# Performance work log

Measured on AMD Instinct MI355X. Metric: run time of the kernel, lower is better.

Reference implementation:

```python
import jax, jax.numpy as jnp
import numpy as np
from jax import lax

B, C, H, W = 8, 96, 192, 192
HEADS = 3
FFN = 2 * C  # chn_expanded * in_channels
EPS = 1e-6


def layernorm2d(x, w, b):
    # channel-mean LayerNorm over dim 1 (NCHW)
    mu = jnp.mean(x, axis=1, keepdims=True)
    var = jnp.mean((x - mu) ** 2, axis=1, keepdims=True)
    y = (x - mu) / jnp.sqrt(var + EPS)
    return w[None, :, None, None] * y + b[None, :, None, None]


def conv1x1(x, w, b):
    # w: [out, in]
    return jnp.einsum('bchw,oc->bohw', x, w) + b[None, :, None, None]


def dwconv3x3(x, w, b):
    # depthwise 3x3, w: [C3, 1, 3, 3]
    y = lax.conv_general_dilated(x, w, (1, 1), 'SAME',
                                 feature_group_count=x.shape[1],
                                 dimension_numbers=('NCHW', 'OIHW', 'NCHW'))
    return y + b[None, :, None, None]


def l2norm(x):
    n = jnp.sqrt(jnp.sum(x * x, axis=-1, keepdims=True))
    return x / jnp.maximum(n, 1e-12)


def setup_inputs() -> dict:
    key = jax.random.key(0)
    ks = jax.random.split(key, 10)
    s = 1.0 / np.sqrt(C)
    return {
        'x': jax.random.normal(ks[0], (B, C, H, W), jnp.float32),
        'ln1_w': jnp.ones((C,), jnp.float32),
        'ln1_b': jnp.zeros((C,), jnp.float32),
        'ln2_w': jnp.ones((C,), jnp.float32),
        'ln2_b': jnp.zeros((C,), jnp.float32),
        'qkv_w': jax.random.normal(ks[1], (3 * C, C), jnp.float32) * s,
        'qkv_b': jnp.zeros((3 * C,), jnp.float32),
        'dw_w': jax.random.normal(ks[2], (3 * C, 1, 3, 3), jnp.float32) * 0.1,
        'dw_b': jnp.zeros((3 * C,), jnp.float32),
        'temp': jnp.ones((HEADS, 1, 1), jnp.float32),
        'proj_w': jax.random.normal(ks[3], (C, C), jnp.float32) * s,
        'proj_b': jnp.zeros((C,), jnp.float32),
        'conv1_w': jax.random.normal(ks[4], (FFN, C), jnp.float32) * s,
        'conv1_b': jnp.zeros((FFN,), jnp.float32),
        'conv2_w': jax.random.normal(ks[5], (C, FFN // 2), jnp.float32) * s,
        'conv2_b': jnp.zeros((C,), jnp.float32),
        'betac': jax.random.normal(ks[6], (1, C, 1, 1), jnp.float32) * 0.1,
        'gamma': jax.random.normal(ks[7], (1, C, 1, 1), jnp.float32) * 0.1,
    }


def channel_attn(qkv, temp, proj_w, proj_b):
    b, c3, h, w = qkv.shape
    q, k, v = jnp.split(qkv, 3, axis=1)
    def r(t):  # b (head c) h w -> b head c (h w)
        return t.reshape(b, HEADS, C // HEADS, h * w)
    q, k, v = r(q), r(k), r(v)
    q = l2norm(q)
    k = l2norm(k)
    attn = jnp.einsum('bhcn,bhdn->bhcd', q, k) * temp[None]  # [b,head,c,c]
    attn = jax.nn.softmax(jax.nn.relu(attn), axis=-1)
    out = jnp.einsum('bhcd,bhdn->bhcn', attn, v)
    out = out.reshape(b, C, h, w)
    return conv1x1(out, proj_w, proj_b)


def reference(x, ln1_w, ln1_b, ln2_w, ln2_b, qkv_w, qkv_b, dw_w, dw_b, temp,
              proj_w, proj_b, conv1_w, conv1_b, conv2_w, conv2_b, betac, gamma):
    xn = layernorm2d(x, ln1_w, ln1_b)
    qkv = dwconv3x3(conv1x1(xn, qkv_w, qkv_b), dw_w, dw_b)
    xc = channel_attn(qkv, temp, proj_w, proj_b)
    y = x + xc * betac
    f = conv1x1(layernorm2d(y, ln2_w, ln2_b), conv1_w, conv1_b)
    f1, f2 = jnp.split(f, 2, axis=1)
    f = conv1x1(f1 * f2, conv2_w, conv2_b)
    return y + f * gamma
```

## Files before the change

### kernel.cpp

```cpp
#include <hip/hip_runtime.h>

#define BB 8
#define C 96
#define HH 192
#define WW 192
#define NPIX (HH*WW)
#define C3 (3*C)
#define NHEADS 3
#define FFND 192
#define EPSV 1e-6f
#define PT 64
#define GNB 768

typedef unsigned short u16;
typedef unsigned int u32;
typedef __attribute__((ext_vector_type(8))) short bf16x8;
typedef __attribute__((ext_vector_type(4))) float f32x4;

__device__ __forceinline__ float b2f(u16 h) {
  u32 u = ((u32)h) << 16;
  return __builtin_bit_cast(float, u);
}
__device__ __forceinline__ u16 f2b(float f) {
  u32 u = __builtin_bit_cast(u32, f);
  u32 r = (u + 0x7FFFu + ((u >> 16) & 1u)) >> 16;
  return (u16)r;
}
__device__ __forceinline__ u32 pk2(float a, float b) {
  return (u32)f2b(a) | ((u32)f2b(b) << 16);
}


__global__ __launch_bounds__(256) void k_prep(
    const float* __restrict__ qkvw, const float* __restrict__ pw,
    const float* __restrict__ c1w, const float* __restrict__ c2w,
    u16* __restrict__ Wf)
{
  int t = blockIdx.x * 256 + threadIdx.x;
  const float* src; u16* dst; int tl;
  if (t < 3456)      { src = qkvw; dst = Wf;         tl = t; }
  else if (t < 4608) { src = pw;   dst = Wf + 27648; tl = t - 3456; }
  else if (t < 6912) { src = c1w;  dst = Wf + 36864; tl = t - 4608; }
  else if (t < 8064) { src = c2w;  dst = Wf + 55296; tl = t - 6912; }
  else return;
  int fid = tl >> 6, lane = tl & 63;
  int mt = fid / 3, kt = fid % 3;
  int row = mt * 16 + (lane & 15), k0 = kt * 32 + (lane >> 4) * 8;
  const float* s = src + row * 96 + k0;
  uint4 v;
  v.x = pk2(s[0], s[1]); v.y = pk2(s[2], s[3]);
  v.z = pk2(s[4], s[5]); v.w = pk2(s[6], s[7]);
  *reinterpret_cast<uint4*>(dst + (size_t)tl * 8) = v;
}

__global__ __launch_bounds__(256) void k_ln1_qkv(
    const float* __restrict__ x, const float* __restrict__ ln1w,
    const float* __restrict__ ln1b, const u16* __restrict__ Wf,
    const float* __restrict__ qb, u16* __restrict__ qkv_pre, int b0)
{
  __shared__ float xs[C][PT + 1];
  __shared__ __align__(16) u16 xt[PT][104];
  __shared__ float mu_s[PT], rs_s[PT];
  __shared__ float lw[C], lb[C];
  const int tid = threadIdx.x;
  const int nt = NPIX / PT;
  const int bl = blockIdx.x / nt;
  const int tile = blockIdx.x % nt;
  const int n0 = tile * PT;
  const float* xb = x + (size_t)(b0 + bl) * C * NPIX + n0;
  for (int i = tid; i < C * PT; i += 256) {
    int c = i >> 6, p = i & 63;
    xs[c][p] = xb[(size_t)c * NPIX + p];
  }
  if (tid < C) { lw[tid] = ln1w[tid]; lb[tid] = ln1b[tid]; }
  __syncthreads();
  float* red = (float*)xt;
  {
    int g = tid >> 6, p = tid & 63;
    float s = 0.f, ss = 0.f;
    for (int c = g * 24; c < g * 24 + 24; c++) { float v = xs[c][p]; s += v; ss += v * v; }
    red[g * 64 + p] = s; red[(4 + g) * 64 + p] = ss;
  }
  __syncthreads();
  if (tid < PT) {
    float s  = red[tid] + red[64 + tid] + red[128 + tid] + red[192 + tid];
    float ss = red[256 + tid] + red[320 + tid] + red[384 + tid] + red[448 + tid];
    float m = s * (1.f / C);
    float var = ss * (1.f / C) - m * m;
    mu_s[tid] = m; rs_s[tid] = rsqrtf(var + EPSV);
  }
  __syncthreads();
  for (int i = tid; i < C * PT; i += 256) {
    int c = i >> 6, p = i & 63;
    xt[p][c] = f2b((xs[c][p] - mu_s[p]) * rs_s[p] * lw[c] + lb[c]);
  }
  __syncthreads();
  const int lane = tid & 63, wv = tid >> 6;
  const int lr = lane & 15, lg = lane >> 4;
  const int pcol = wv * 16 + lr;
  bf16x8 bf[3];
  #pragma unroll
  for (int kt = 0; kt < 3; kt++)
    bf[kt] = *reinterpret_cast<const bf16x8*>(&xt[pcol][kt * 32 + lg * 8]);
  const bf16x8* wfp = reinterpret_cast<const bf16x8*>(Wf);
  u16* outb = qkv_pre + (size_t)bl * C3 * NPIX + n0 + pcol;
  for (int mt = 0; mt < 18; mt++) {
    f32x4 acc = {0.f, 0.f, 0.f, 0.f};
    #pragma unroll
    for (int kt = 0; kt < 3; kt++)
      acc = __builtin_amdgcn_mfma_f32_16x16x32_bf16(wfp[(mt * 3 + kt) * 64 + lane], bf[kt], acc, 0, 0, 0);
    #pragma unroll
    for (int r = 0; r < 4; r++) {
      int o = mt * 16 + lg * 4 + r;
      outb[(size_t)o * NPIX] = f2b(acc[r] + qb[o]);
    }
  }
}

__global__ __launch_bounds__(256) void k_dwconv(
    const u16* __restrict__ src, const float* __restrict__ dww,
    const float* __restrict__ dwb, u16* __restrict__ dst)
{
  long qid = (long)blockIdx.x * 256 + threadIdx.x;
  int wq = (int)(qid % 48);
  long t = qid / 48;
  int h = (int)(t % HH); t /= HH;
  int ch = (int)(t % C3);
  int bl = (int)(t / C3);
  const u16* p = src + ((size_t)bl * C3 + ch) * NPIX;
  float wgt[9];
  #pragma unroll
  for (int i = 0; i < 9; i++) wgt[i] = dww[ch * 9 + i];
  float acc0 = 0.f, acc1 = 0.f, acc2 = 0.f, acc3 = 0.f;
  int w0 = wq * 4;
  #pragma unroll
  for (int dh = -1; dh <= 1; dh++) {
    int hh = h + dh;
    if (hh < 0 || hh >= HH) continue;
    const u16* row = p + (size_t)hh * WW;
    ushort4 v4 = *reinterpret_cast<const ushort4*>(row + w0);
    float r0 = (w0 > 0) ? b2f(row[w0 - 1]) : 0.f;
    float r1 = b2f(v4.x), r2 = b2f(v4.y), r3 = b2f(v4.z), r4v = b2f(v4.w);
    float r5 = (w0 + 4 < WW) ? b2f(row[w0 + 4]) : 0.f;
    float wA = wgt[(dh + 1) * 3 + 0];
    float wB = wgt[(dh + 1) * 3 + 1];
    float wC = wgt[(dh + 1) * 3 + 2];
    acc0 += r0 * wA + r1 * wB + r2 * wC;
    acc1 += r1 * wA + r2 * wB + r3 * wC;
    acc2 += r2 * wA + r3 * wB + r4v * wC;
    acc3 += r3 * wA + r4v * wB + r5 * wC;
  }
  float bb = dwb[ch];
  ushort4 o4;
  o4.x = f2b(acc0 + bb); o4.y = f2b(acc1 + bb);
  o4.z = f2b(acc2 + bb); o4.w = f2b(acc3 + bb);
  *reinterpret_cast<ushort4*>(dst + ((size_t)bl * C3 + ch) * NPIX + (size_t)h * WW + w0) = o4;
}

__global__ __launch_bounds__(256) void k_gram(
    const u16* __restrict__ qkv, float* __restrict__ G,
    float* __restrict__ nq, float* __restrict__ nk, int b0)
{
  __shared__ float gred[4][1024];
  const int tid = threadIdx.x, lane = tid & 63, wv = tid >> 6;
  const int nch = NPIX / GNB;
  const int bhl = blockIdx.x / nch;
  const int chunk = blockIdx.x % nch;
  const int bl = bhl / NHEADS, hd = bhl % NHEADS;
  const int bh = (b0 + bl) * NHEADS + hd;
  const int lr = lane & 15, lg = lane >> 4;
  const u16* qb_ = qkv + ((size_t)bl * C3 + hd * 32) * NPIX;
  const u16* kb_ = qkv + ((size_t)bl * C3 + C + hd * 32) * NPIX;
  const int nbase = chunk * GNB + wv * (GNB / 4);
  f32x4 a00 = {0,0,0,0}, a01 = {0,0,0,0}, a10 = {0,0,0,0}, a11 = {0,0,0,0};
  float sq0 = 0.f, sq1 = 0.f, sk0 = 0.f, sk1 = 0.f;
  #pragma unroll 2
  for (int it = 0; it < GNB / 4 / 32; it++) {
    int n = nbase + it * 32 + lg * 8;
    bf16x8 fa0 = *reinterpret_cast<const bf16x8*>(qb_ + (size_t)lr * NPIX + n);
    bf16x8 fa1 = *reinterpret_cast<const bf16x8*>(qb_ + (size_t)(16 + lr) * NPIX + n);
    bf16x8 fb0 = *reinterpret_cast<const bf16x8*>(kb_ + (size_t)lr * NPIX + n);
    bf16x8 fb1 = *reinterpret_cast<const bf16x8*>(kb_ + (size_t)(16 + lr) * NPIX + n);
    a00 = __builtin_amdgcn_mfma_f32_16x16x32_bf16(fa0, fb0, a00, 0, 0, 0);
    a01 = __builtin_amdgcn_mfma_f32_16x16x32_bf16(fa0, fb1, a01, 0, 0, 0);
    a10 = __builtin_amdgcn_mfma_f32_16x16x32_bf16(fa1, fb0, a10, 0, 0, 0);
    a11 = __builtin_amdgcn_mfma_f32_16x16x32_bf16(fa1, fb1, a11, 0, 0, 0);
    #pragma unroll
    for (int j = 0; j < 8; j++) {
      float q0 = b2f((u16)fa0[j]), q1 = b2f((u16)fa1[j]);
      float k0 = b2f((u16)fb0[j]), k1 = b2f((u16)fb1[j]);
      sq0 += q0 * q0; sq1 += q1 * q1; sk0 += k0 * k0; sk1 += k1 * k1;
    }
  }
  #pragma unroll
  for (int r = 0; r < 4; r++) {
    gred[wv][(0  + lg * 4 + r) * 32 + 0  + lr] = a00[r];
    gred[wv][(0  + lg * 4 + r) * 32 + 16 + lr] = a01[r];
    gred[wv][(16 + lg * 4 + r) * 32 + 0  + lr] = a10[r];
    gred[wv][(16 + lg * 4 + r) * 32 + 16 + lr] = a11[r];
  }
  sq0 += __shfl_xor(sq0, 16); sq0 += __shfl_xor(sq0, 32);
  sq1 += __shfl_xor(sq1, 16); sq1 += __shfl_xor(sq1, 32);
  sk0 += __shfl_xor(sk0, 16); sk0 += __shfl_xor(sk0, 32);
  sk1 += __shfl_xor(sk1, 16); sk1 += __shfl_xor(sk1, 32);
  if (lg == 0) {
    atomicAdd(&nq[bh * 32 + lr], sq0);
    atomicAdd(&nq[bh * 32 + 16 + lr], sq1);
    atomicAdd(&nk[bh * 32 + lr], sk0);
    atomicAdd(&nk[bh * 32 + 16 + lr], sk1);
  }
  __syncthreads();
  for (int i = tid; i < 1024; i += 256) {
    float s = gred[0][i] + gred[1][i] + gred[2][i] + gred[3][i];
    atomicAdd(&G[(size_t)bh * 1024 + i], s);
  }
}

__global__ void k_softmax(const float* __restrict__ G, const float* __restrict__ nq,
                          const float* __restrict__ nk, const float* __restrict__ temp,
                          u16* __restrict__ Af, int b0)
{
  int bh = b0 * NHEADS + blockIdx.x;
  int c = threadIdx.x;
  int hd = bh % NHEADS;
  float tmp = temp[hd];
  float nqc = fmaxf(sqrtf(nq[bh * 32 + c]), 1e-12f);
  float a[32];
  float m = 0.f;
  #pragma unroll
  for (int d = 0; d < 32; d++) {
    float nkd = fmaxf(sqrtf(nk[bh * 32 + d]), 1e-12f);
    float v = G[(size_t)bh * 1024 + c * 32 + d] / (nqc * nkd) * tmp;
    v = fmaxf(v, 0.f);
    a[d] = v; m = fmaxf(m, v);
  }
  float s = 0.f;
  #pragma unroll
  for (int d = 0; d < 32; d++) { a[d] = expf(a[d] - m); s += a[d]; }
  float inv = 1.f / s;
  #pragma unroll
  for (int lg = 0; lg < 4; lg++) {
    uint4 v;
    v.x = pk2(a[8 * lg + 0] * inv, a[8 * lg + 1] * inv);
    v.y = pk2(a[8 * lg + 2] * inv, a[8 * lg + 3] * inv);
    v.z = pk2(a[8 * lg + 4] * inv, a[8 * lg + 5] * inv);
    v.w = pk2(a[8 * lg + 6] * inv, a[8 * lg + 7] * inv);
    *reinterpret_cast<uint4*>(Af + ((size_t)(bh * 2 + (c >> 4)) * 64 + lg * 16 + (c & 15)) * 8) = v;
  }
}

__global__ __launch_bounds__(256) void k_av_proj(
    const u16* __restrict__ qkv, const u16* __restrict__ Af,
    const u16* __restrict__ pWf, const float* __restrict__ pb,
    const float* __restrict__ x, const float* __restrict__ betac,
    float* __restrict__ y, int b0)
{
  __shared__ __align__(16) u16 vt[PT][104];
  __shared__ __align__(16) u16 avt[PT][104];
  const int tid = threadIdx.x;
  const int nt = NPIX / PT;
  const int bl = blockIdx.x / nt;
  const int tile = blockIdx.x % nt;
  const int b = b0 + bl;
  const int n0 = tile * PT;
  const u16* vb = qkv + ((size_t)bl * C3 + 2 * C) * NPIX + n0;
  for (int i = tid; i < C * PT; i += 256) {
    int c = i >> 6, p = i & 63;
    vt[p][c] = vb[(size_t)c * NPIX + p];
  }
  __syncthreads();
  const int lane = tid & 63, wv = tid >> 6;
  const int lr = lane & 15, lg = lane >> 4;
  const int pcol = wv * 16 + lr;
  const bf16x8* afp = reinterpret_cast<const bf16x8*>(Af);
  #pragma unroll
  for (int h = 0; h < NHEADS; h++) {
    bf16x8 bv = *reinterpret_cast<const bf16x8*>(&vt[pcol][h * 32 + lg * 8]);
    #pragma unroll
    for (int mt = 0; mt < 2; mt++) {
      f32x4 acc = {0.f, 0.f, 0.f, 0.f};
      acc = __builtin_amdgcn_mfma_f32_16x16x32_bf16(
          afp[((size_t)(b * NHEADS + h) * 2 + mt) * 64 + lane], bv, acc, 0, 0, 0);
      int o = h * 32 + mt * 16 + lg * 4;
      u32* dst = reinterpret_cast<u32*>(&avt[pcol][o]);
      dst[0] = pk2(acc[0], acc[1]);
      dst[1] = pk2(acc[2], acc[3]);
    }
  }
  bf16x8 ba[3];
  #pragma unroll
  for (int kt = 0; kt < 3; kt++)
    ba[kt] = *reinterpret_cast<const bf16x8*>(&avt[pcol][kt * 32 + lg * 8]);
  const bf16x8* pwp = reinterpret_cast<const bf16x8*>(pWf);
  const float* xb = x + (size_t)b * C * NPIX + n0 + pcol;
  float* yb = y + (size_t)b * C * NPIX + n0 + pcol;
  for (int mt = 0; mt < 6; mt++) {
    f32x4 acc = {0.f, 0.f, 0.f, 0.f};
    #pragma unroll
    for (int kt = 0; kt < 3; kt++)
      acc = __builtin_amdgcn_mfma_f32_16x16x32_bf16(pwp[(mt * 3 + kt) * 64 + lane], ba[kt], acc, 0, 0, 0);
    #pragma unroll
    for (int r = 0; r < 4; r++) {
      int o = mt * 16 + lg * 4 + r;
      yb[(size_t)o * NPIX] = xb[(size_t)o * NPIX] + (acc[r] + pb[o]) * betac[o];
    }
  }
}

__global__ __launch_bounds__(256) void k_ffn(
    float* __restrict__ y, const float* __restrict__ ln2w,
    const float* __restrict__ ln2b, const u16* __restrict__ c1f,
    const u16* __restrict__ c2f, const float* __restrict__ c1b,
    const float* __restrict__ c2b, const float* __restrict__ gamma)
{
  __shared__ float xs[C][PT + 1];
  __shared__ __align__(16) u16 yt[PT][104];
  __shared__ __align__(16) u16 gt[PT][104];
  __shared__ float mu_s[PT], rs_s[PT];
  __shared__ float lw[C], lb[C];
  const int tid = threadIdx.x;
  const int nt = NPIX / PT;
  const int b = blockIdx.x / nt;
  const int tile = blockIdx.x % nt;
  const int n0 = tile * PT;
  float* yb = y + (size_t)b * C * NPIX + n0;
  for (int i = tid; i < C * PT; i += 256) {
    int c = i >> 6, p = i & 63;
    xs[c][p] = yb[(size_t)c * NPIX + p];
  }
  if (tid < C) { lw[tid] = ln2w[tid]; lb[tid] = ln2b[tid]; }
  __syncthreads();
  float* red = (float*)yt;
  {
    int g = tid >> 6, p = tid & 63;
    float s = 0.f, ss = 0.f;
    for (int c = g * 24; c < g * 24 + 24; c++) { float v = xs[c][p]; s += v; ss += v * v; }
    red[g * 64 + p] = s; red[(4 + g) * 64 + p] = ss;
  }
  __syncthreads();
  if (tid < PT) {
    float s  = red[tid] + red[64 + tid] + red[128 + tid] + red[192 + tid];
    float ss = red[256 + tid] + red[320 + tid] + red[384 + tid] + red[448 + tid];
    float m = s * (1.f / C);
    float var = ss * (1.f / C) - m * m;
    mu_s[tid] = m; rs_s[tid] = rsqrtf(var + EPSV);
  }
  __syncthreads();
  for (int i = tid; i < C * PT; i += 256) {
    int c = i >> 6, p = i & 63;
    yt[p][c] = f2b((xs[c][p] - mu_s[p]) * rs_s[p] * lw[c] + lb[c]);
  }
  __syncthreads();
  const int lane = tid & 63, wv = tid >> 6;
  const int lr = lane & 15, lg = lane >> 4;
  const int pcol = wv * 16 + lr;
  bf16x8 by[3];
  #pragma unroll
  for (int kt = 0; kt < 3; kt++)
    by[kt] = *reinterpret_cast<const bf16x8*>(&yt[pcol][kt * 32 + lg * 8]);
  const bf16x8* w1 = reinterpret_cast<const bf16x8*>(c1f);
  const bf16x8* w2 = reinterpret_cast<const bf16x8*>(c2f);
  for (int mt = 0; mt < 6; mt++) {
    f32x4 a1 = {0.f, 0.f, 0.f, 0.f}, a2 = {0.f, 0.f, 0.f, 0.f};
    #pragma unroll
    for (int kt = 0; kt < 3; kt++) {
      a1 = __builtin_amdgcn_mfma_f32_16x16x32_bf16(w1[(mt * 3 + kt) * 64 + lane], by[kt], a1, 0, 0, 0);
      a2 = __builtin_amdgcn_mfma_f32_16x16x32_bf16(w1[((mt + 6) * 3 + kt) * 64 + lane], by[kt], a2, 0, 0, 0);
    }
    int o = mt * 16 + lg * 4;
    float g0 = (a1[0] + c1b[o + 0]) * (a2[0] + c1b[o + 96]);
    float g1 = (a1[1] + c1b[o + 1]) * (a2[1] + c1b[o + 97]);
    float g2 = (a1[2] + c1b[o + 2]) * (a2[2] + c1b[o + 98]);
    float g3 = (a1[3] + c1b[o + 3]) * (a2[3] + c1b[o + 99]);
    u32* dst = reinterpret_cast<u32*>(&gt[pcol][o]);
    dst[0] = pk2(g0, g1);
    dst[1] = pk2(g2, g3);
  }
  bf16x8 bg[3];
  #pragma unroll
  for (int kt = 0; kt < 3; kt++)
    bg[kt] = *reinterpret_cast<const bf16x8*>(&gt[pcol][kt * 32 + lg * 8]);
  for (int mt = 0; mt < 6; mt++) {
    f32x4 acc = {0.f, 0.f, 0.f, 0.f};
    #pragma unroll
    for (int kt = 0; kt < 3; kt++)
      acc = __builtin_amdgcn_mfma_f32_16x16x32_bf16(w2[(mt * 3 + kt) * 64 + lane], bg[kt], acc, 0, 0, 0);
    #pragma unroll
    for (int r = 0; r < 4; r++) {
      int o = mt * 16 + lg * 4 + r;
      yb[(size_t)o * NPIX + pcol] = xs[o][pcol] + (acc[r] + c2b[o]) * gamma[o];
    }
  }
}

extern "C" void kernel_launch(void* const* d_in, const int* in_sizes, int n_in,
                              void* d_out, int out_size, void* d_ws, size_t ws_size,
                              hipStream_t stream)
{
  const float* x     = (const float*)d_in[0];
  const float* ln1w  = (const float*)d_in[1];
  const float* ln1b  = (const float*)d_in[2];
  const float* ln2w  = (const float*)d_in[3];
  const float* ln2b  = (const float*)d_in[4];
  const float* qkvw  = (const float*)d_in[5];
  const float* qkvb  = (const float*)d_in[6];
  const float* dww   = (const float*)d_in[7];
  const float* dwb   = (const float*)d_in[8];
  const float* temp  = (const float*)d_in[9];
  const float* pw    = (const float*)d_in[10];
  const float* pb    = (const float*)d_in[11];
  const float* c1w   = (const float*)d_in[12];
  const float* c1b   = (const float*)d_in[13];
  const float* c2w   = (const float*)d_in[14];
  const float* c2b   = (const float*)d_in[15];
  const float* betac = (const float*)d_in[16];
  const float* gamma = (const float*)d_in[17];
  float* out = (float*)d_out;

  char* ws = (char*)d_ws;
  size_t off = 0;
  float* G  = (float*)(ws + off); off += (size_t)BB * NHEADS * 1024 * sizeof(float);
  float* nq = (float*)(ws + off); off += (size_t)BB * NHEADS * 32 * sizeof(float);
  float* nk = (float*)(ws + off); off += (size_t)BB * NHEADS * 32 * sizeof(float);
  u16* Af   = (u16*)(ws + off);   off += (size_t)BB * NHEADS * 2 * 64 * 8 * sizeof(u16);
  u16* Wf   = (u16*)(ws + off);   off += (size_t)64512 * sizeof(u16);
  off = (off + 255) & ~(size_t)255;

  const size_t per_batch = 2 * (size_t)C3 * NPIX * sizeof(u16);
  int cb = 8;
  while (cb > 1 && off + (size_t)cb * per_batch > ws_size) cb >>= 1;
  if (off + (size_t)cb * per_batch > ws_size) return;
  u16* qkv_pre = (u16*)(ws + off);
  u16* qkvq    = qkv_pre + (size_t)cb * C3 * NPIX;

  const u16* projWf = Wf + 27648;
  const u16* c1f    = Wf + 36864;
  const u16* c2f    = Wf + 55296;

  hipMemsetAsync(G, 0, (size_t)(BB * NHEADS * 1024 + 2 * BB * NHEADS * 32) * sizeof(float),
                 stream);
  k_prep<<<32, 256, 0, stream>>>(qkvw, pw, c1w, c2w, Wf);

  for (int b0 = 0; b0 < BB; b0 += cb) {
    k_ln1_qkv<<<cb * (NPIX / PT), 256, 0, stream>>>(x, ln1w, ln1b, Wf, qkvb, qkv_pre, b0);
    long quads = (long)cb * C3 * HH * (WW / 4);
    k_dwconv<<<(int)(quads / 256), 256, 0, stream>>>(qkv_pre, dww, dwb, qkvq);
    k_gram<<<cb * NHEADS * (NPIX / GNB), 256, 0, stream>>>(qkvq, G, nq, nk, b0);
    k_softmax<<<cb * NHEADS, 32, 0, stream>>>(G, nq, nk, temp, Af, b0);
    k_av_proj<<<cb * (NPIX / PT), 256, 0, stream>>>(qkvq, Af, projWf, pb, x, betac, out, b0);
  }

  k_ffn<<<BB * (NPIX / PT), 256, 0, stream>>>(out, ln2w, ln2b, c1f, c2f, c1b, c2b, gamma);
}
```

Before: 718.1 us.

## Swap MFMA operands for vector stores and tile depthwise conv through LDS

The three 1x1-conv GEMM epilogues (qkv, proj, ffn conv2) swap the MFMA A/B operands so each lane holds four consecutive pixels of one output channel. They can then write packed bf16x4 or float4 vectors instead of four scalar strided stores. The depthwise 3x3 conv is rewritten to stage a 34-row band of one channel into LDS, with each thread producing 8 outputs from 16-byte loads. This cuts redundant global reads and narrow stores, at the cost of LDS use and a block-level sync.

```diff
diff --git a/kernel.cpp b/kernel.cpp
--- a/kernel.cpp
+++ b/kernel.cpp
@@ -11,6 +11,7 @@
 #define EPSV 1e-6f
 #define PT 64
 #define GNB 768
+#define DWR 32
 
 typedef unsigned short u16;
 typedef unsigned int u32;
@@ -103,17 +104,18 @@
   for (int kt = 0; kt < 3; kt++)
     bf[kt] = *reinterpret_cast<const bf16x8*>(&xt[pcol][kt * 32 + lg * 8]);
   const bf16x8* wfp = reinterpret_cast<const bf16x8*>(Wf);
-  u16* outb = qkv_pre + (size_t)bl * C3 * NPIX + n0 + pcol;
+  u16* outb = qkv_pre + (size_t)bl * C3 * NPIX + n0 + wv * 16 + lg * 4;
   for (int mt = 0; mt < 18; mt++) {
     f32x4 acc = {0.f, 0.f, 0.f, 0.f};
     #pragma unroll
     for (int kt = 0; kt < 3; kt++)
-      acc = __builtin_amdgcn_mfma_f32_16x16x32_bf16(wfp[(mt * 3 + kt) * 64 + lane], bf[kt], acc, 0, 0, 0);
-    #pragma unroll
-    for (int r = 0; r < 4; r++) {
-      int o = mt * 16 + lg * 4 + r;
-      outb[(size_t)o * NPIX] = f2b(acc[r] + qb[o]);
-    }
+      acc = __builtin_amdgcn_mfma_f32_16x16x32_bf16(bf[kt], wfp[(mt * 3 + kt) * 64 + lane], acc, 0, 0, 0);
+    int o = mt * 16 + lr;
+    float bv = qb[o];
+    uint2 pk;
+    pk.x = pk2(acc[0] + bv, acc[1] + bv);
+    pk.y = pk2(acc[2] + bv, acc[3] + bv);
+    *reinterpret_cast<uint2*>(outb + (size_t)o * NPIX) = pk;
   }
 }
 
@@ -121,40 +123,56 @@
     const u16* __restrict__ src, const float* __restrict__ dww,
     const float* __restrict__ dwb, u16* __restrict__ dst)
 {
-  long qid = (long)blockIdx.x * 256 + threadIdx.x;
-  int wq = (int)(qid % 48);
-  long t = qid / 48;
-  int h = (int)(t % HH); t /= HH;
-  int ch = (int)(t % C3);
-  int bl = (int)(t / C3);
+  const int ch = blockIdx.x, band = blockIdx.y, bl = blockIdx.z;
+  const int tid = threadIdx.x;
   const u16* p = src + ((size_t)bl * C3 + ch) * NPIX;
+  u16* q = dst + ((size_t)bl * C3 + ch) * NPIX;
+  const int h0 = band * DWR;
+  __shared__ __align__(16) u16 rows[(DWR + 2) * 200];
+  for (int i = tid; i < (DWR + 2) * 24; i += 256) {
+    int r = i / 24, seg = i % 24;
+    int h = h0 - 1 + r;
+    uint4 v = {0u, 0u, 0u, 0u};
+    if (h >= 0 && h < HH)
+      v = *reinterpret_cast<const uint4*>(p + (size_t)h * WW + seg * 8);
+    *reinterpret_cast<uint4*>(&rows[r * 200 + seg * 8]) = v;
+  }
   float wgt[9];
   #pragma unroll
   for (int i = 0; i < 9; i++) wgt[i] = dww[ch * 9 + i];
-  float acc0 = 0.f, acc1 = 0.f, acc2 = 0.f, acc3 = 0.f;
-  int w0 = wq * 4;
-  #pragma unroll
-  for (int dh = -1; dh <= 1; dh++) {
-    int hh = h + dh;
-    if (hh < 0 || hh >= HH) continue;
-    const u16* row = p + (size_t)hh * WW;
-    ushort4 v4 = *reinterpret_cast<const ushort4*>(row + w0);
-    float r0 = (w0 > 0) ? b2f(row[w0 - 1]) : 0.f;
-    float r1 = b2f(v4.x), r2 = b2f(v4.y), r3 = b2f(v4.z), r4v = b2f(v4.w);
-    float r5 = (w0 + 4 < WW) ? b2f(row[w0 + 4]) : 0.f;
-    float wA = wgt[(dh + 1) * 3 + 0];
-    float wB = wgt[(dh + 1) * 3 + 1];
-    float wC = wgt[(dh + 1) * 3 + 2];
-    acc0 += r0 * wA + r1 * wB + r2 * wC;
-    acc1 += r1 * wA + r2 * wB + r3 * wC;
-    acc2 += r2 * wA + r3 * wB + r4v * wC;
-    acc3 += r3 * wA + r4v * wB + r5 * wC;
-  }
-  float bb = dwb[ch];
-  ushort4 o4;
-  o4.x = f2b(acc0 + bb); o4.y = f2b(acc1 + bb);
-  o4.z = f2b(acc2 + bb); o4.w = f2b(acc3 + bb);
-  *reinterpret_cast<ushort4*>(dst + ((size_t)bl * C3 + ch) * NPIX + (size_t)h * WW + w0) = o4;
+  const float bias = dwb[ch];
+  __syncthreads();
+  #pragma unroll
+  for (int it = 0; it < 3; it++) {
+    int i = it * 256 + tid;
+    int r = i / 24, seg = i % 24;
+    float o0 = bias, o1 = bias, o2 = bias, o3 = bias;
+    float o4 = bias, o5 = bias, o6 = bias, o7 = bias;
+    #pragma unroll
+    for (int dr = 0; dr < 3; dr++) {
+      const u16* rp = &rows[(r + dr) * 200 + seg * 8];
+      uint4 cv = *reinterpret_cast<const uint4*>(rp);
+      float c0 = b2f((u16)(cv.x & 0xffff)), c1 = b2f((u16)(cv.x >> 16));
+      float c2 = b2f((u16)(cv.y & 0xffff)), c3 = b2f((u16)(cv.y >> 16));
+      float c4 = b2f((u16)(cv.z & 0xffff)), c5 = b2f((u16)(cv.z >> 16));
+      float c6 = b2f((u16)(cv.w & 0xffff)), c7 = b2f((u16)(cv.w >> 16));
+      float lf = (seg > 0)  ? b2f(rp[-1]) : 0.f;
+      float rg = (seg < 23) ? b2f(rp[8])  : 0.f;
+      float wA = wgt[dr * 3 + 0], wB = wgt[dr * 3 + 1], wC = wgt[dr * 3 + 2];
+      o0 += lf * wA + c0 * wB + c1 * wC;
+      o1 += c0 * wA + c1 * wB + c2 * wC;
+      o2 += c1 * wA + c2 * wB + c3 * wC;
+      o3 += c2 * wA + c3 * wB + c4 * wC;
+      o4 += c3 * wA + c4 * wB + c5 * wC;
+      o5 += c4 * wA + c5 * wB + c6 * wC;
+      o6 += c5 * wA + c6 * wB + c7 * wC;
+      o7 += c6 * wA + c7 * wB + rg * wC;
+    }
+    uint4 ov;
+    ov.x = pk2(o0, o1); ov.y = pk2(o2, o3);
+    ov.z = pk2(o4, o5); ov.w = pk2(o6, o7);
+    *reinterpret_cast<uint4*>(q + (size_t)(h0 + r) * WW + seg * 8) = ov;
+  }
 }
 
 __global__ __launch_bounds__(256) void k_gram(
@@ -292,18 +310,22 @@
   for (int kt = 0; kt < 3; kt++)
     ba[kt] = *reinterpret_cast<const bf16x8*>(&avt[pcol][kt * 32 + lg * 8]);
   const bf16x8* pwp = reinterpret_cast<const bf16x8*>(pWf);
-  const float* xb = x + (size_t)b * C * NPIX + n0 + pcol;
-  float* yb = y + (size_t)b * C * NPIX + n0 + pcol;
+  const float* xb = x + (size_t)b * C * NPIX + n0 + wv * 16 + lg * 4;
+  float* yb = y + (size_t)b * C * NPIX + n0 + wv * 16 + lg * 4;
   for (int mt = 0; mt < 6; mt++) {
     f32x4 acc = {0.f, 0.f, 0.f, 0.f};
     #pragma unroll
     for (int kt = 0; kt < 3; kt++)
-      acc = __builtin_amdgcn_mfma_f32_16x16x32_bf16(pwp[(mt * 3 + kt) * 64 + lane], ba[kt], acc, 0, 0, 0);
-    #pragma unroll
-    for (int r = 0; r < 4; r++) {
-      int o = mt * 16 + lg * 4 + r;
-      yb[(size_t)o * NPIX] = xb[(size_t)o * NPIX] + (acc[r] + pb[o]) * betac[o];
-    }
+      acc = __builtin_amdgcn_mfma_f32_16x16x32_bf16(ba[kt], pwp[(mt * 3 + kt) * 64 + lane], acc, 0, 0, 0);
+    int o = mt * 16 + lr;
+    float bv = pb[o], bt = betac[o];
+    float4 xv = *reinterpret_cast<const float4*>(xb + (size_t)o * NPIX);
+    float4 yv;
+    yv.x = xv.x + (acc[0] + bv) * bt;
+    yv.y = xv.y + (acc[1] + bv) * bt;
+    yv.z = xv.z + (acc[2] + bv) * bt;
+    yv.w = xv.w + (acc[3] + bv) * bt;
+    *reinterpret_cast<float4*>(yb + (size_t)o * NPIX) = yv;
   }
 }
 
@@ -380,16 +402,20 @@
   #pragma unroll
   for (int kt = 0; kt < 3; kt++)
     bg[kt] = *reinterpret_cast<const bf16x8*>(&gt[pcol][kt * 32 + lg * 8]);
+  const int pix = wv * 16 + lg * 4;
   for (int mt = 0; mt < 6; mt++) {
     f32x4 acc = {0.f, 0.f, 0.f, 0.f};
     #pragma unroll
     for (int kt = 0; kt < 3; kt++)
-      acc = __builtin_amdgcn_mfma_f32_16x16x32_bf16(w2[(mt * 3 + kt) * 64 + lane], bg[kt], acc, 0, 0, 0);
-    #pragma unroll
-    for (int r = 0; r < 4; r++) {
-      int o = mt * 16 + lg * 4 + r;
-      yb[(size_t)o * NPIX + pcol] = xs[o][pcol] + (acc[r] + c2b[o]) * gamma[o];
-    }
+      acc = __builtin_amdgcn_mfma_f32_16x16x32_bf16(bg[kt], w2[(mt * 3 + kt) * 64 + lane], acc, 0, 0, 0);
+    int o = mt * 16 + lr;
+    float g = gamma[o], cb2 = c2b[o];
+    float4 ov;
+    ov.x = xs[o][pix + 0] + (acc[0] + cb2) * g;
+    ov.y = xs[o][pix + 1] + (acc[1] + cb2) * g;
+    ov.z = xs[o][pix + 2] + (acc[2] + cb2) * g;
+    ov.w = xs[o][pix + 3] + (acc[3] + cb2) * g;
+    *reinterpret_cast<float4*>(yb + (size_t)o * NPIX + pix) = ov;
   }
 }
 
@@ -443,8 +469,7 @@
 
   for (int b0 = 0; b0 < BB; b0 += cb) {
     k_ln1_qkv<<<cb * (NPIX / PT), 256, 0, stream>>>(x, ln1w, ln1b, Wf, qkvb, qkv_pre, b0);
-    long quads = (long)cb * C3 * HH * (WW / 4);
-    k_dwconv<<<(int)(quads / 256), 256, 0, stream>>>(qkv_pre, dww, dwb, qkvq);
+    k_dwconv<<<dim3(C3, HH / DWR, cb), 256, 0, stream>>>(qkv_pre, dww, dwb, qkvq);
     k_gram<<<cb * NHEADS * (NPIX / GNB), 256, 0, stream>>>(qkvq, G, nq, nk, b0);
     k_softmax<<<cb * NHEADS, 32, 0, stream>>>(G, nq, nk, temp, Af, b0);
     k_av_proj<<<cb * (NPIX / PT), 256, 0, stream>>>(qkvq, Af, projWf, pb, x, betac, out, b0);
```

Result: faster. 588.0 us (-18.1%).
